# Optimization experiments

Hardware: AMD Instinct MI355X
Metric: run time of the kernel (lower is better)

Reference implementation:

```python
import jax, jax.numpy as jnp
import numpy as np

B, S, H = 64, 2048, 1024

def setup_inputs() -> dict:
    key = jax.random.key(0)
    k1, k2, k3, k4, k5 = jax.random.split(key, 5)
    scale = 1.0 / np.sqrt(H)
    return {
        "dec_hidden": jax.random.normal(k1, (B, 1, H), dtype=jnp.float32),
        "enc_outputs": jax.random.normal(k2, (B, S, H), dtype=jnp.float32),
        "W_h": jax.random.normal(k3, (H, H), dtype=jnp.float32) * scale,
        "W_s": jax.random.normal(k4, (H, H), dtype=jnp.float32) * scale,
        "v": jax.random.normal(k5, (H,), dtype=jnp.float32) * scale,
    }

def reference(dec_hidden, enc_outputs, W_h, W_s, v):
    # energy = tanh(enc @ W_h^T + dec @ W_s^T)  -> [B, S, H]
    enc_proj = jnp.einsum('bsh,oh->bso', enc_outputs, W_h)
    dec_proj = jnp.einsum('bqh,oh->bqo', dec_hidden, W_s)  # [B,1,H]
    energy = jnp.tanh(enc_proj + dec_proj)
    # score = energy @ v -> [B, S]
    score = jnp.einsum('bsh,h->bs', energy, v)
    weights = jax.nn.softmax(score, axis=-1)
    # context = weights[:, None, :] @ enc_outputs -> [B, 1, H]
    context = jnp.einsum('bs,bsh->bh', weights, enc_outputs)[:, None, :]
    return (context, weights)
```

## Files before the change

### kernel.cpp

```cpp
#include <hip/hip_runtime.h>
#include <hip/hip_bf16.h>


#define B_ 64
#define S_ 2048
#define H_ 1024

typedef __attribute__((ext_vector_type(8))) short short8;
typedef __attribute__((ext_vector_type(4))) float floatx4;

__device__ __forceinline__ short f2bf(float f) {
    unsigned u = __float_as_uint(f);
    return (short)((u + 0x7FFFu + ((u >> 16) & 1u)) >> 16);
}
__device__ __forceinline__ unsigned pk2bf(float a, float b) {
    unsigned ua = __float_as_uint(a), ub = __float_as_uint(b);
    ua = (ua + 0x7FFFu + ((ua >> 16) & 1u)) >> 16;
    ub = (ub + 0x7FFFu + ((ub >> 16) & 1u)) & 0xFFFF0000u;
    return ua | ub;
}
__device__ __forceinline__ void gload_lds16(const void* g, void* l) {
    __builtin_amdgcn_global_load_lds(
        (const __attribute__((address_space(1))) unsigned*)g,
        (__attribute__((address_space(3))) unsigned*)l, 16, 0, 0);
}

__global__ __launch_bounds__(256) void zero_score_kernel(float* __restrict__ sc) {
    ((float4*)sc)[blockIdx.x * 256 + threadIdx.x] = make_float4(0.f, 0.f, 0.f, 0.f);
}

__global__ __launch_bounds__(256) void dec_proj_kernel(
        const float* __restrict__ dec, const float* __restrict__ Ws,
        float* __restrict__ dp) {
    __shared__ float sdec[H_];
    const int b = blockIdx.y;
    const int o = blockIdx.x * 256 + threadIdx.x;
    ((float4*)sdec)[threadIdx.x] = ((const float4*)(dec + b * H_))[threadIdx.x];
    __syncthreads();
    const float4* wr = (const float4*)(Ws + (size_t)o * H_);
    float acc = 0.f;
#pragma unroll 4
    for (int i = 0; i < H_ / 4; ++i) {
        float4 wv = wr[i];
        acc += sdec[4*i+0]*wv.x + sdec[4*i+1]*wv.y + sdec[4*i+2]*wv.z + sdec[4*i+3]*wv.w;
    }
    dp[b * H_ + o] = acc;
}

__global__ __launch_bounds__(256) void cvt_wh_kernel(
        const float* __restrict__ Wh, short* __restrict__ Wbf) {
    const int i = blockIdx.x * 256 + threadIdx.x;
    float4 f = ((const float4*)Wh)[i];
    *(short4*)&Wbf[i * 4] = make_short4(f2bf(f.x), f2bf(f.y), f2bf(f.z), f2bf(f.w));
}

__global__ __launch_bounds__(256) void cvt_enc_kernel(
        const float* __restrict__ enc, short* __restrict__ out) {
    const size_t total = (size_t)B_ * S_ * H_ / 8;
    for (size_t c = (size_t)blockIdx.x * 256 + threadIdx.x; c < total;
         c += (size_t)gridDim.x * 256) {
        const float4* p = (const float4*)enc + c * 2;
        float4 f0 = p[0], f1 = p[1];
        union { short8 s; unsigned u[4]; } cv;
        cv.u[0] = pk2bf(f0.x, f0.y);
        cv.u[1] = pk2bf(f0.z, f0.w);
        cv.u[2] = pk2bf(f1.x, f1.y);
        cv.u[3] = pk2bf(f1.z, f1.w);
        ((short8*)out)[c] = cv.s;
    }
}

template<int USE_BF>
__global__ __launch_bounds__(256, 3) void score_kernel(
        const float* __restrict__ enc, const short* __restrict__ encbf,
        const short* __restrict__ Wbf, const float* __restrict__ dp,
        const float* __restrict__ v, float* __restrict__ score) {
    __shared__ short As[128 * 64];
    __shared__ short Bs[128 * 64];

    const int tid  = threadIdx.x;
    const int wave = tid >> 6;
    const int lane = tid & 63;
    const int l15  = lane & 15;
    const int quad = lane >> 4;
    const int wy   = wave & 1;
    const int wx   = wave >> 1;

    const int mtile = blockIdx.x >> 3;
    const int nb    = blockIdx.x & 7;
    const int m0    = mtile * 128;
    const int n0    = nb * 128;
    const int b     = m0 >> 11;

    floatx4 acc[4][4];
#pragma unroll
    for (int i = 0; i < 4; ++i)
#pragma unroll
        for (int j = 0; j < 4; ++j) acc[i][j] = (floatx4){0.f, 0.f, 0.f, 0.f};

    const short* aLds = As + (wy * 64 + l15) * 64;
    const short* bLds = Bs + (wx * 64 + l15) * 64;
    const int swz = l15 & 7;

    const int srow = tid >> 3;
    const int bc   = tid & 7;

    for (int k0 = 0; k0 < H_; k0 += 64) {
#pragma unroll
        for (int r = 0; r < 4; ++r) {
            const int n = r * 32 + srow;
            const int g = bc ^ (n & 7);
            const short* gp = Wbf + (size_t)(n0 + n) * H_ + k0 + g * 8;
            gload_lds16(gp, (void*)(Bs + (r * 256 + wave * 64) * 8));
        }
        if (USE_BF) {
#pragma unroll
            for (int r = 0; r < 4; ++r) {
                const int m = r * 32 + srow;
                const int g = bc ^ (m & 7);
                const short* gp = encbf + (size_t)(m0 + m) * H_ + k0 + g * 8;
                gload_lds16(gp, (void*)(As + (r * 256 + wave * 64) * 8));
            }
        } else {
#pragma unroll
            for (int i = 0; i < 4; ++i) {
                const int La = i * 256 + tid;
                const int m  = La >> 3;
                const int c8 = La & 7;
                const float4* gp = (const float4*)(enc + (size_t)(m0 + m) * H_ + k0 + c8 * 8);
                float4 f0 = gp[0], f1 = gp[1];
                union { short8 s; unsigned u[4]; } cv;
                cv.u[0] = pk2bf(f0.x, f0.y);
                cv.u[1] = pk2bf(f0.z, f0.w);
                cv.u[2] = pk2bf(f1.x, f1.y);
                cv.u[3] = pk2bf(f1.z, f1.w);
                *(short8*)&As[m * 64 + (c8 ^ (m & 7)) * 8] = cv.s;
            }
        }
        __syncthreads();

#pragma unroll
        for (int kt = 0; kt < 2; ++kt) {
            short8 af[4], bfr[4];
#pragma unroll
            for (int i = 0; i < 4; ++i)
                af[i] = *(const short8*)(aLds + i * 16 * 64 + (((kt * 4 + quad) ^ swz) * 8));
#pragma unroll
            for (int j = 0; j < 4; ++j)
                bfr[j] = *(const short8*)(bLds + j * 16 * 64 + (((kt * 4 + quad) ^ swz) * 8));
#pragma unroll
            for (int i = 0; i < 4; ++i)
#pragma unroll
                for (int j = 0; j < 4; ++j)
                    acc[i][j] = __builtin_amdgcn_mfma_f32_16x16x32_bf16(af[i], bfr[j], acc[i][j], 0, 0, 0);
        }
        __syncthreads();
    }

    float part[4][4];
#pragma unroll
    for (int i = 0; i < 4; ++i)
#pragma unroll
        for (int r = 0; r < 4; ++r) part[i][r] = 0.f;

#pragma unroll
    for (int j = 0; j < 4; ++j) {
        const int o = n0 + wx * 64 + j * 16 + l15;
        const float dpv = dp[b * H_ + o];
        const float vv  = v[o];
#pragma unroll
        for (int i = 0; i < 4; ++i)
#pragma unroll
            for (int r = 0; r < 4; ++r) {
                float x = acc[i][j][r] + dpv;
                x = fminf(10.f, fmaxf(-10.f, x));
                float e = __expf(x + x);
                float t = 1.f - 2.f * __builtin_amdgcn_rcpf(e + 1.f);
                part[i][r] += t * vv;
            }
    }
#pragma unroll
    for (int i = 0; i < 4; ++i)
#pragma unroll
        for (int r = 0; r < 4; ++r) {
            float s = part[i][r];
            s += __shfl_xor(s, 1, 64);
            s += __shfl_xor(s, 2, 64);
            s += __shfl_xor(s, 4, 64);
            s += __shfl_xor(s, 8, 64);
            if (l15 == 0)
                atomicAdd(&score[m0 + wy * 64 + i * 16 + quad * 4 + r], s);
        }
}

__global__ __launch_bounds__(256) void softmax_kernel(float* __restrict__ out) {
    const int b = blockIdx.x;
    const int tid = threadIdx.x;
    float* sc = out + B_ * H_ + b * S_;

    ((float4*)(out + b * H_))[tid] = make_float4(0.f, 0.f, 0.f, 0.f);

    float xs[8];
    float m = -1e30f;
#pragma unroll
    for (int i = 0; i < 8; ++i) { xs[i] = sc[tid + i * 256]; m = fmaxf(m, xs[i]); }
#pragma unroll
    for (int off = 32; off > 0; off >>= 1) m = fmaxf(m, __shfl_xor(m, off, 64));
    __shared__ float redm[4];
    const int wv = tid >> 6;
    if ((tid & 63) == 0) redm[wv] = m;
    __syncthreads();
    m = fmaxf(fmaxf(redm[0], redm[1]), fmaxf(redm[2], redm[3]));

    float s = 0.f;
#pragma unroll
    for (int i = 0; i < 8; ++i) { xs[i] = __expf(xs[i] - m); s += xs[i]; }
#pragma unroll
    for (int off = 32; off > 0; off >>= 1) s += __shfl_xor(s, off, 64);
    __shared__ float reds[4];
    if ((tid & 63) == 0) reds[wv] = s;
    __syncthreads();
    s = reds[0] + reds[1] + reds[2] + reds[3];

    const float inv = 1.f / s;
#pragma unroll
    for (int i = 0; i < 8; ++i) sc[tid + i * 256] = xs[i] * inv;
}

__global__ __launch_bounds__(256) void context_kernel(
        const float* __restrict__ enc, const float* __restrict__ wts,
        float* __restrict__ ctx) {
    const int b    = blockIdx.x;
    const int scnk = blockIdx.y;
    const int t    = threadIdx.x;
    const float* w  = wts + b * S_ + scnk * 256;
    const float4* e = (const float4*)(enc + ((long)b * S_ + scnk * 256) * H_);
    float4 acc = make_float4(0.f, 0.f, 0.f, 0.f);
#pragma unroll 4
    for (int s = 0; s < 256; ++s) {
        const float ww = w[s];
        const float4 ev = e[s * (H_ / 4) + t];
        acc.x = fmaf(ww, ev.x, acc.x);
        acc.y = fmaf(ww, ev.y, acc.y);
        acc.z = fmaf(ww, ev.z, acc.z);
        acc.w = fmaf(ww, ev.w, acc.w);
    }
    float* c = ctx + b * H_ + t * 4;
    atomicAdd(c + 0, acc.x);
    atomicAdd(c + 1, acc.y);
    atomicAdd(c + 2, acc.z);
    atomicAdd(c + 3, acc.w);
}

extern "C" void kernel_launch(void* const* d_in, const int* in_sizes, int n_in,
                              void* d_out, int out_size, void* d_ws, size_t ws_size,
                              hipStream_t stream) {
    const float* dec = (const float*)d_in[0];
    const float* enc = (const float*)d_in[1];
    const float* Wh  = (const float*)d_in[2];
    const float* Ws  = (const float*)d_in[3];
    const float* v   = (const float*)d_in[4];

    float* out = (float*)d_out;
    float* ctx = out;
    float* wts = out + B_ * H_;

    float* dp  = (float*)d_ws;
    short* Wbf = (short*)((char*)d_ws + (size_t)B_ * H_ * 4);
    const size_t base = (size_t)B_ * H_ * 4 + (size_t)H_ * H_ * 2;
    const size_t enc_need = (size_t)B_ * S_ * H_ * 2;
    short* encbf = (ws_size >= base + enc_need)
                       ? (short*)((char*)d_ws + base) : nullptr;
    (void)in_sizes; (void)n_in; (void)out_size;

    zero_score_kernel<<<(B_ * S_ / 4) / 256, 256, 0, stream>>>(wts);
    dec_proj_kernel<<<dim3(H_ / 256, B_), 256, 0, stream>>>(dec, Ws, dp);
    cvt_wh_kernel<<<(H_ * H_ / 4) / 256, 256, 0, stream>>>(Wh, Wbf);
    if (encbf) {
        cvt_enc_kernel<<<8192, 256, 0, stream>>>(enc, encbf);
        score_kernel<1><<<(B_ * S_ / 128) * (H_ / 128), 256, 0, stream>>>(
            enc, encbf, Wbf, dp, v, wts);
    } else {
        score_kernel<0><<<(B_ * S_ / 128) * (H_ / 128), 256, 0, stream>>>(
            enc, nullptr, Wbf, dp, v, wts);
    }
    softmax_kernel<<<B_, 256, 0, stream>>>(out);
    context_kernel<<<dim3(B_, S_ / 256), 256, 0, stream>>>(enc, wts, ctx);
}
```

Measured before the change: 1.157 ms.

## Replace score GEMM with 256x256-tile, 512-thread, double-buffered pipelined kernel

The bf16 score GEMM now uses 256x256 output tiles with 8 waves per block. A and B tiles are double-buffered in LDS, and the next k-tile's global-to-LDS loads are interleaved with MFMA phases using explicit barriers, waitcnt and setprio. This targets the exposed global-load latency and the low operand reuse of the 128x128 single-buffered kernel. In exchange it uses more LDS and registers per block (acc[8][4]), which may limit occupancy and makes the hand-written wait counts fragile. The fp32 fallback path is kept as a separate kernel.

```diff
diff --git a/kernel.cpp b/kernel.cpp
--- a/kernel.cpp
+++ b/kernel.cpp
@@ -5,6 +5,7 @@
 #define B_ 64
 #define S_ 2048
 #define H_ 1024
+#define NT_ 16
 
 typedef __attribute__((ext_vector_type(8))) short short8;
 typedef __attribute__((ext_vector_type(4))) float floatx4;
@@ -70,13 +71,55 @@
     }
 }
 
-template<int USE_BF>
-__global__ __launch_bounds__(256, 3) void score_kernel(
-        const float* __restrict__ enc, const short* __restrict__ encbf,
-        const short* __restrict__ Wbf, const float* __restrict__ dp,
-        const float* __restrict__ v, float* __restrict__ score) {
-    __shared__ short As[128 * 64];
-    __shared__ short Bs[128 * 64];
+#define STAGEA(bufp, half, ktile) do {                                          \
+    gload_lds16(gA + (size_t)(half) * (128 * H_) + (ktile) * 64,                \
+                &As[(bufp)][(half)][wave * 512]);                               \
+    gload_lds16(gA + (size_t)(half) * (128 * H_) + (ktile) * 64 + 64 * H_,      \
+                &As[(bufp)][(half)][4096 + wave * 512]);                        \
+} while (0)
+#define STAGEB(bufp, half, ktile) do {                                          \
+    gload_lds16(gB + (size_t)(half) * (128 * H_) + (ktile) * 64,                \
+                &Bs[(bufp)][(half)][wave * 512]);                               \
+    gload_lds16(gB + (size_t)(half) * (128 * H_) + (ktile) * 64 + 64 * H_,      \
+                &Bs[(bufp)][(half)][4096 + wave * 512]);                        \
+} while (0)
+
+#define MFMA16(I0) do {                                                         \
+    _Pragma("unroll")                                                           \
+    for (int kt = 0; kt < 2; ++kt) {                                            \
+        _Pragma("unroll")                                                       \
+        for (int j = 0; j < 4; ++j) {                                           \
+            acc[I0][j]     = __builtin_amdgcn_mfma_f32_16x16x32_bf16(           \
+                                 af[0][kt], bfr[kt][j], acc[I0][j], 0, 0, 0);   \
+            acc[(I0)+1][j] = __builtin_amdgcn_mfma_f32_16x16x32_bf16(           \
+                                 af[1][kt], bfr[kt][j], acc[(I0)+1][j], 0, 0, 0); \
+        }                                                                       \
+    }                                                                           \
+} while (0)
+
+#define PHASE(I0, STG, TAILWAIT) do {                                           \
+    _Pragma("unroll")                                                           \
+    for (int ii = 0; ii < 2; ++ii)                                              \
+        _Pragma("unroll")                                                       \
+        for (int kt = 0; kt < 2; ++kt)                                          \
+            af[ii][kt] = *(const short8*)(aBase + ((I0) + ii) * 1024 +          \
+                                          (((kt * 4 + quad) ^ swz) * 8));       \
+    STG;                                                                        \
+    __builtin_amdgcn_s_barrier();                                               \
+    asm volatile("s_waitcnt lgkmcnt(0)" ::: "memory");                          \
+    __builtin_amdgcn_s_setprio(1);                                              \
+    MFMA16(I0);                                                                 \
+    __builtin_amdgcn_s_setprio(0);                                              \
+    TAILWAIT;                                                                   \
+    __builtin_amdgcn_s_barrier();                                               \
+} while (0)
+
+__global__ __launch_bounds__(512, 2) void score256_kernel(
+        const short* __restrict__ encbf, const short* __restrict__ Wbf,
+        const float* __restrict__ dp, const float* __restrict__ v,
+        float* __restrict__ score) {
+    __shared__ short As[2][2][128 * 64];
+    __shared__ short Bs[2][2][128 * 64];
 
     const int tid  = threadIdx.x;
     const int wave = tid >> 6;
@@ -86,6 +129,105 @@
     const int wy   = wave & 1;
     const int wx   = wave >> 1;
 
+    const int mtile = blockIdx.x >> 2;
+    const int nb    = blockIdx.x & 3;
+    const int m0    = mtile * 256;
+    const int n0    = nb * 256;
+    const int b     = m0 >> 11;
+    const int swz   = l15 & 7;
+
+    const int rr0 = tid >> 3;
+    const int g8  = (tid & 7) ^ (rr0 & 7);
+    const short* gA = encbf + (size_t)(m0 + rr0) * H_ + g8 * 8;
+    const short* gB = Wbf   + (size_t)(n0 + rr0) * H_ + g8 * 8;
+
+    floatx4 acc[8][4];
+#pragma unroll
+    for (int i = 0; i < 8; ++i)
+#pragma unroll
+        for (int j = 0; j < 4; ++j) acc[i][j] = (floatx4){0.f, 0.f, 0.f, 0.f};
+
+    short8 af[2][2];
+    short8 bfr[2][4];
+
+    STAGEA(0, 0, 0); STAGEA(0, 1, 0);
+    STAGEB(0, 0, 0); STAGEB(0, 1, 0);
+    STAGEB(1, 0, 1); STAGEB(1, 1, 1);
+    asm volatile("s_waitcnt vmcnt(4)" ::: "memory");
+    __builtin_amdgcn_s_barrier();
+
+#pragma unroll 1
+    for (int t = 0; t < NT_; ++t) {
+        const int buf = t & 1;
+        const short* aBase = &As[buf][wy][0] + l15 * 64;
+        const short* bBase = &Bs[buf][wx >> 1][0] + ((wx & 1) * 64 + l15) * 64;
+
+#pragma unroll
+        for (int kt = 0; kt < 2; ++kt)
+#pragma unroll
+            for (int j = 0; j < 4; ++j)
+                bfr[kt][j] = *(const short8*)(bBase + j * 1024 +
+                                              (((kt * 4 + quad) ^ swz) * 8));
+
+        PHASE(0, { if (t + 1 < NT_) STAGEA(buf ^ 1, 0, t + 1); }, (void)0);
+        PHASE(2, { if (t + 1 < NT_) STAGEA(buf ^ 1, 1, t + 1); }, (void)0);
+        PHASE(4, { if (t + 2 < NT_) STAGEB(buf, 0, t + 2); }, (void)0);
+        PHASE(6, { if (t + 2 < NT_) STAGEB(buf, 1, t + 2); },
+              { if (t < NT_ - 2) { asm volatile("s_waitcnt vmcnt(4)" ::: "memory"); }
+                else             { asm volatile("s_waitcnt vmcnt(0)" ::: "memory"); } });
+    }
+
+    float part[8][4];
+#pragma unroll
+    for (int i = 0; i < 8; ++i)
+#pragma unroll
+        for (int r = 0; r < 4; ++r) part[i][r] = 0.f;
+
+#pragma unroll
+    for (int j = 0; j < 4; ++j) {
+        const int o = n0 + wx * 64 + j * 16 + l15;
+        const float dpv = dp[b * H_ + o];
+        const float vv  = v[o];
+#pragma unroll
+        for (int i = 0; i < 8; ++i)
+#pragma unroll
+            for (int r = 0; r < 4; ++r) {
+                float x = acc[i][j][r] + dpv;
+                x = fminf(10.f, fmaxf(-10.f, x));
+                float e = __expf(x + x);
+                float t = 1.f - 2.f * __builtin_amdgcn_rcpf(e + 1.f);
+                part[i][r] += t * vv;
+            }
+    }
+#pragma unroll
+    for (int i = 0; i < 8; ++i)
+#pragma unroll
+        for (int r = 0; r < 4; ++r) {
+            float s = part[i][r];
+            s += __shfl_xor(s, 1, 64);
+            s += __shfl_xor(s, 2, 64);
+            s += __shfl_xor(s, 4, 64);
+            s += __shfl_xor(s, 8, 64);
+            if (l15 == 0)
+                atomicAdd(&score[m0 + wy * 128 + i * 16 + quad * 4 + r], s);
+        }
+}
+
+__global__ __launch_bounds__(256, 3) void score_kernel_fb(
+        const float* __restrict__ enc, const short* __restrict__ Wbf,
+        const float* __restrict__ dp, const float* __restrict__ v,
+        float* __restrict__ score) {
+    __shared__ short As[128 * 64];
+    __shared__ short Bs[128 * 64];
+
+    const int tid  = threadIdx.x;
+    const int wave = tid >> 6;
+    const int lane = tid & 63;
+    const int l15  = lane & 15;
+    const int quad = lane >> 4;
+    const int wy   = wave & 1;
+    const int wx   = wave >> 1;
+
     const int mtile = blockIdx.x >> 3;
     const int nb    = blockIdx.x & 7;
     const int m0    = mtile * 128;
@@ -101,7 +243,6 @@
     const short* aLds = As + (wy * 64 + l15) * 64;
     const short* bLds = Bs + (wx * 64 + l15) * 64;
     const int swz = l15 & 7;
-
     const int srow = tid >> 3;
     const int bc   = tid & 7;
 
@@ -113,46 +254,35 @@
             const short* gp = Wbf + (size_t)(n0 + n) * H_ + k0 + g * 8;
             gload_lds16(gp, (void*)(Bs + (r * 256 + wave * 64) * 8));
         }
-        if (USE_BF) {
-#pragma unroll
-            for (int r = 0; r < 4; ++r) {
-                const int m = r * 32 + srow;
-                const int g = bc ^ (m & 7);
-                const short* gp = encbf + (size_t)(m0 + m) * H_ + k0 + g * 8;
-                gload_lds16(gp, (void*)(As + (r * 256 + wave * 64) * 8));
-            }
-        } else {
-#pragma unroll
-            for (int i = 0; i < 4; ++i) {
-                const int La = i * 256 + tid;
-                const int m  = La >> 3;
-                const int c8 = La & 7;
-                const float4* gp = (const float4*)(enc + (size_t)(m0 + m) * H_ + k0 + c8 * 8);
-                float4 f0 = gp[0], f1 = gp[1];
-                union { short8 s; unsigned u[4]; } cv;
-                cv.u[0] = pk2bf(f0.x, f0.y);
-                cv.u[1] = pk2bf(f0.z, f0.w);
-                cv.u[2] = pk2bf(f1.x, f1.y);
-                cv.u[3] = pk2bf(f1.z, f1.w);
-                *(short8*)&As[m * 64 + (c8 ^ (m & 7)) * 8] = cv.s;
-            }
+#pragma unroll
+        for (int i = 0; i < 4; ++i) {
+            const int La = i * 256 + tid;
+            const int m  = La >> 3;
+            const int c8 = La & 7;
+            const float4* gp = (const float4*)(enc + (size_t)(m0 + m) * H_ + k0 + c8 * 8);
+            float4 f0 = gp[0], f1 = gp[1];
+            union { short8 s; unsigned u[4]; } cv;
+            cv.u[0] = pk2bf(f0.x, f0.y);
+            cv.u[1] = pk2bf(f0.z, f0.w);
+            cv.u[2] = pk2bf(f1.x, f1.y);
+            cv.u[3] = pk2bf(f1.z, f1.w);
+            *(short8*)&As[m * 64 + (c8 ^ (m & 7)) * 8] = cv.s;
         }
         __syncthreads();
-
 #pragma unroll
         for (int kt = 0; kt < 2; ++kt) {
-            short8 af[4], bfr[4];
+            short8 a2[4], b2[4];
 #pragma unroll
             for (int i = 0; i < 4; ++i)
-                af[i] = *(const short8*)(aLds + i * 16 * 64 + (((kt * 4 + quad) ^ swz) * 8));
+                a2[i] = *(const short8*)(aLds + i * 16 * 64 + (((kt * 4 + quad) ^ swz) * 8));
 #pragma unroll
             for (int j = 0; j < 4; ++j)
-                bfr[j] = *(const short8*)(bLds + j * 16 * 64 + (((kt * 4 + quad) ^ swz) * 8));
+                b2[j] = *(const short8*)(bLds + j * 16 * 64 + (((kt * 4 + quad) ^ swz) * 8));
 #pragma unroll
             for (int i = 0; i < 4; ++i)
 #pragma unroll
                 for (int j = 0; j < 4; ++j)
-                    acc[i][j] = __builtin_amdgcn_mfma_f32_16x16x32_bf16(af[i], bfr[j], acc[i][j], 0, 0, 0);
+                    acc[i][j] = __builtin_amdgcn_mfma_f32_16x16x32_bf16(a2[i], b2[j], acc[i][j], 0, 0, 0);
         }
         __syncthreads();
     }
@@ -162,7 +292,6 @@
     for (int i = 0; i < 4; ++i)
 #pragma unroll
         for (int r = 0; r < 4; ++r) part[i][r] = 0.f;
-
 #pragma unroll
     for (int j = 0; j < 4; ++j) {
         const int o = n0 + wx * 64 + j * 16 + l15;
@@ -278,11 +407,11 @@
     cvt_wh_kernel<<<(H_ * H_ / 4) / 256, 256, 0, stream>>>(Wh, Wbf);
     if (encbf) {
         cvt_enc_kernel<<<8192, 256, 0, stream>>>(enc, encbf);
-        score_kernel<1><<<(B_ * S_ / 128) * (H_ / 128), 256, 0, stream>>>(
-            enc, encbf, Wbf, dp, v, wts);
+        score256_kernel<<<(B_ * S_ / 256) * (H_ / 256), 512, 0, stream>>>(
+            encbf, Wbf, dp, v, wts);
     } else {
-        score_kernel<0><<<(B_ * S_ / 128) * (H_ / 128), 256, 0, stream>>>(
-            enc, nullptr, Wbf, dp, v, wts);
+        score_kernel_fb<<<(B_ * S_ / 128) * (H_ / 128), 256, 0, stream>>>(
+            enc, Wbf, dp, v, wts);
     }
     softmax_kernel<<<B_, 256, 0, stream>>>(out);
     context_kernel<<<dim3(B_, S_ / 256), 256, 0, stream>>>(enc, wts, ctx);
```

New measurement: 1.198 ms. 3.6% more time.

## Fuse fp32-to-bf16 encoder conversion into score GEMM via fp32 LDS staging

Applied to the files above, without the earlier changes.

Removes the separate pass that converted the whole encoder tensor to bf16 in workspace. The score kernel now streams fp32 encoder tiles straight into LDS with direct global-to-LDS loads and converts them to bf16 at fragment-load time using the hardware packed convert instruction. This avoids writing and re-reading a large bf16 copy of the encoder. In exchange, the A tile doubles LDS footprint and global traffic per tile, and the conversion ALU work is repeated for each of the 8 column blocks.

```diff
diff --git a/kernel.cpp b/kernel.cpp
--- a/kernel.cpp
+++ b/kernel.cpp
@@ -13,11 +13,10 @@
     unsigned u = __float_as_uint(f);
     return (short)((u + 0x7FFFu + ((u >> 16) & 1u)) >> 16);
 }
-__device__ __forceinline__ unsigned pk2bf(float a, float b) {
-    unsigned ua = __float_as_uint(a), ub = __float_as_uint(b);
-    ua = (ua + 0x7FFFu + ((ua >> 16) & 1u)) >> 16;
-    ub = (ub + 0x7FFFu + ((ub >> 16) & 1u)) & 0xFFFF0000u;
-    return ua | ub;
+__device__ __forceinline__ unsigned cvtpk(float a, float b) {
+    unsigned r;
+    asm("v_cvt_pk_bf16_f32 %0, %1, %2" : "=v"(r) : "v"(a), "v"(b));
+    return r;
 }
 __device__ __forceinline__ void gload_lds16(const void* g, void* l) {
     __builtin_amdgcn_global_load_lds(
@@ -54,28 +53,11 @@
     *(short4*)&Wbf[i * 4] = make_short4(f2bf(f.x), f2bf(f.y), f2bf(f.z), f2bf(f.w));
 }
 
-__global__ __launch_bounds__(256) void cvt_enc_kernel(
-        const float* __restrict__ enc, short* __restrict__ out) {
-    const size_t total = (size_t)B_ * S_ * H_ / 8;
-    for (size_t c = (size_t)blockIdx.x * 256 + threadIdx.x; c < total;
-         c += (size_t)gridDim.x * 256) {
-        const float4* p = (const float4*)enc + c * 2;
-        float4 f0 = p[0], f1 = p[1];
-        union { short8 s; unsigned u[4]; } cv;
-        cv.u[0] = pk2bf(f0.x, f0.y);
-        cv.u[1] = pk2bf(f0.z, f0.w);
-        cv.u[2] = pk2bf(f1.x, f1.y);
-        cv.u[3] = pk2bf(f1.z, f1.w);
-        ((short8*)out)[c] = cv.s;
-    }
-}
-
-template<int USE_BF>
-__global__ __launch_bounds__(256, 3) void score_kernel(
-        const float* __restrict__ enc, const short* __restrict__ encbf,
-        const short* __restrict__ Wbf, const float* __restrict__ dp,
-        const float* __restrict__ v, float* __restrict__ score) {
-    __shared__ short As[128 * 64];
+__global__ __launch_bounds__(256, 3) void score128_kernel(
+        const float* __restrict__ enc, const short* __restrict__ Wbf,
+        const float* __restrict__ dp, const float* __restrict__ v,
+        float* __restrict__ score) {
+    __shared__ float Asf[128 * 64];
     __shared__ short Bs[128 * 64];
 
     const int tid  = threadIdx.x;
@@ -98,61 +80,50 @@
 #pragma unroll
         for (int j = 0; j < 4; ++j) acc[i][j] = (floatx4){0.f, 0.f, 0.f, 0.f};
 
-    const short* aLds = As + (wy * 64 + l15) * 64;
-    const short* bLds = Bs + (wx * 64 + l15) * 64;
     const int swz = l15 & 7;
 
-    const int srow = tid >> 3;
-    const int bc   = tid & 7;
+    const int bn  = tid >> 3;
+    const short* gB0 = Wbf + (size_t)(n0 + bn) * H_ + ((tid & 7) ^ (bn & 7)) * 8;
+    const int an  = tid >> 4;
+    const float* gA0 = enc + (size_t)(m0 + an) * H_ + (((tid & 15) ^ an) << 2);
+
+    const float4* aRow = (const float4*)Asf + (wy * 64 + l15) * 16;
+    const short*  bLds = Bs + (wx * 64 + l15) * 64;
 
     for (int k0 = 0; k0 < H_; k0 += 64) {
 #pragma unroll
-        for (int r = 0; r < 4; ++r) {
-            const int n = r * 32 + srow;
-            const int g = bc ^ (n & 7);
-            const short* gp = Wbf + (size_t)(n0 + n) * H_ + k0 + g * 8;
-            gload_lds16(gp, (void*)(Bs + (r * 256 + wave * 64) * 8));
-        }
-        if (USE_BF) {
-#pragma unroll
-            for (int r = 0; r < 4; ++r) {
-                const int m = r * 32 + srow;
-                const int g = bc ^ (m & 7);
-                const short* gp = encbf + (size_t)(m0 + m) * H_ + k0 + g * 8;
-                gload_lds16(gp, (void*)(As + (r * 256 + wave * 64) * 8));
+        for (int r = 0; r < 4; ++r)
+            gload_lds16(gB0 + (size_t)r * 32 * H_ + k0,
+                        (void*)(Bs + (r * 256 + wave * 64) * 8));
+#pragma unroll
+        for (int r = 0; r < 8; ++r)
+            gload_lds16(gA0 + (size_t)r * 16 * H_ + k0,
+                        (void*)(Asf + (r * 256 + wave * 64) * 4));
+        __syncthreads();
+
+#pragma unroll
+        for (int kt = 0; kt < 2; ++kt) {
+            const int c0 = 8 * kt + 2 * quad;
+            short8 a2[4], b2[4];
+#pragma unroll
+            for (int i = 0; i < 4; ++i) {
+                float4 f0 = aRow[i * 256 + (c0 ^ l15)];
+                float4 f1 = aRow[i * 256 + ((c0 + 1) ^ l15)];
+                union { short8 s; unsigned u[4]; } cv;
+                cv.u[0] = cvtpk(f0.x, f0.y);
+                cv.u[1] = cvtpk(f0.z, f0.w);
+                cv.u[2] = cvtpk(f1.x, f1.y);
+                cv.u[3] = cvtpk(f1.z, f1.w);
+                a2[i] = cv.s;
             }
-        } else {
-#pragma unroll
-            for (int i = 0; i < 4; ++i) {
-                const int La = i * 256 + tid;
-                const int m  = La >> 3;
-                const int c8 = La & 7;
-                const float4* gp = (const float4*)(enc + (size_t)(m0 + m) * H_ + k0 + c8 * 8);
-                float4 f0 = gp[0], f1 = gp[1];
-                union { short8 s; unsigned u[4]; } cv;
-                cv.u[0] = pk2bf(f0.x, f0.y);
-                cv.u[1] = pk2bf(f0.z, f0.w);
-                cv.u[2] = pk2bf(f1.x, f1.y);
-                cv.u[3] = pk2bf(f1.z, f1.w);
-                *(short8*)&As[m * 64 + (c8 ^ (m & 7)) * 8] = cv.s;
-            }
-        }
-        __syncthreads();
-
-#pragma unroll
-        for (int kt = 0; kt < 2; ++kt) {
-            short8 af[4], bfr[4];
+#pragma unroll
+            for (int j = 0; j < 4; ++j)
+                b2[j] = *(const short8*)(bLds + j * 1024 + (((kt * 4 + quad) ^ swz) * 8));
 #pragma unroll
             for (int i = 0; i < 4; ++i)
-                af[i] = *(const short8*)(aLds + i * 16 * 64 + (((kt * 4 + quad) ^ swz) * 8));
-#pragma unroll
-            for (int j = 0; j < 4; ++j)
-                bfr[j] = *(const short8*)(bLds + j * 16 * 64 + (((kt * 4 + quad) ^ swz) * 8));
-#pragma unroll
-            for (int i = 0; i < 4; ++i)
 #pragma unroll
                 for (int j = 0; j < 4; ++j)
-                    acc[i][j] = __builtin_amdgcn_mfma_f32_16x16x32_bf16(af[i], bfr[j], acc[i][j], 0, 0, 0);
+                    acc[i][j] = __builtin_amdgcn_mfma_f32_16x16x32_bf16(a2[i], b2[j], acc[i][j], 0, 0, 0);
         }
         __syncthreads();
     }
@@ -267,23 +238,13 @@
 
     float* dp  = (float*)d_ws;
     short* Wbf = (short*)((char*)d_ws + (size_t)B_ * H_ * 4);
-    const size_t base = (size_t)B_ * H_ * 4 + (size_t)H_ * H_ * 2;
-    const size_t enc_need = (size_t)B_ * S_ * H_ * 2;
-    short* encbf = (ws_size >= base + enc_need)
-                       ? (short*)((char*)d_ws + base) : nullptr;
-    (void)in_sizes; (void)n_in; (void)out_size;
+    (void)in_sizes; (void)n_in; (void)out_size; (void)ws_size;
 
     zero_score_kernel<<<(B_ * S_ / 4) / 256, 256, 0, stream>>>(wts);
     dec_proj_kernel<<<dim3(H_ / 256, B_), 256, 0, stream>>>(dec, Ws, dp);
     cvt_wh_kernel<<<(H_ * H_ / 4) / 256, 256, 0, stream>>>(Wh, Wbf);
-    if (encbf) {
-        cvt_enc_kernel<<<8192, 256, 0, stream>>>(enc, encbf);
-        score_kernel<1><<<(B_ * S_ / 128) * (H_ / 128), 256, 0, stream>>>(
-            enc, encbf, Wbf, dp, v, wts);
-    } else {
-        score_kernel<0><<<(B_ * S_ / 128) * (H_ / 128), 256, 0, stream>>>(
-            enc, nullptr, Wbf, dp, v, wts);
-    }
+    score128_kernel<<<(B_ * S_ / 128) * (H_ / 128), 256, 0, stream>>>(
+        enc, Wbf, dp, v, wts);
     softmax_kernel<<<B_, 256, 0, stream>>>(out);
     context_kernel<<<dim3(B_, S_ / 256), 256, 0, stream>>>(enc, wts, ctx);
 }
```

Result: slower. 1.240 ms (+7.2%).
